# Optimization experiments

Measured on AMD Instinct MI355X. Metric: run time of the kernel, lower is better.

The kernel has to match this reference:

```python
import jax, jax.numpy as jnp
import numpy as np

B, D, M, H = 512, 2048, 128, 128
INIT_SCALE = 0.02

def setup_inputs() -> dict:
    key = jax.random.key(0)
    k_x, k_w1, k_w2 = jax.random.split(key, 3)
    return {
        "pre_activation_history": jax.random.normal(k_x, (B, D, M), dtype=jnp.float32),
        # conv1: grouped Conv1d(D -> D*H, kernel=M, groups=D) == per-channel W1[d]: [H, M]
        "W1": jax.random.normal(k_w1, (D, H, M), dtype=jnp.float32) * INIT_SCALE,
        "b1": jnp.zeros((D, H), dtype=jnp.float32),
        # linear_out: grouped 1x1 Conv1d(D*H -> D, groups=D) == per-channel w2[d]: [H]
        "W2": jax.random.normal(k_w2, (D, H), dtype=jnp.float32) * INIT_SCALE,
        "b2": jnp.zeros((D,), dtype=jnp.float32),
    }

def reference(pre_activation_history, W1, b1, W2, b2):
    # per-neuron MLP: [B,D,M] x [D,H,M] -> [B,D,H]
    h = jnp.einsum("bdm,dhm->bdh", pre_activation_history, W1) + b1
    g = jax.nn.gelu(h, approximate=False)  # torch F.gelu default = exact erf
    out = jnp.einsum("bdh,dh->bd", g, W2) + b2  # [B, D]
    return out
```

## Files before the change

kernel.cpp:

```cpp
#include <hip/hip_runtime.h>
#include <hip/hip_bf16.h>
#include <math.h>

#define B_SZ 512
#define D_SZ 2048
#define M_SZ 128
#define H_SZ 128
#define BCHUNK 64
#define NCHUNKS (B_SZ / BCHUNK)

typedef __attribute__((ext_vector_type(8))) short bf16x8;
typedef __attribute__((ext_vector_type(4))) float f32x4;
typedef __attribute__((ext_vector_type(4))) unsigned short us4;

__device__ __forceinline__ unsigned short f2bf(float f) {
    unsigned u = __builtin_bit_cast(unsigned, f);
    u += 0x7fffu + ((u >> 16) & 1u);
    return (unsigned short)(u >> 16);
}

__device__ __forceinline__ float gelu_fast(float h) {
    float u = h * h;
    float z = h * fmaf(0.0713548162726f, u, 1.5957691216057308f);
    float e = __expf(-z);
    return __fdividef(h, 1.0f + e);
}

__global__ __launch_bounds__(256, 3) void nlm_kernel(
    const float* __restrict__ x,
    const float* __restrict__ W1,
    const float* __restrict__ b1,
    const float* __restrict__ W2,
    const float* __restrict__ b2,
    float* __restrict__ out)
{
    __shared__ __align__(16) unsigned short W1s[H_SZ * M_SZ];
    __shared__ __align__(16) unsigned short Xs[BCHUNK * M_SZ];

    const int bid = blockIdx.x;
    const int d = (bid & 7) * 256 + (bid >> 3);

    const int tid  = threadIdx.x;
    const int l    = tid & 63;
    const int w    = tid >> 6;
    const int lrow = l & 15;
    const int lk   = l >> 4;
    const int swz  = (lrow & 7) << 4;

    const float* W1d = W1 + (size_t)d * (H_SZ * M_SZ);
    #pragma unroll
    for (int i = 0; i < 16; ++i) {
        int idx = tid + i * 256;
        int r = idx >> 5, c4 = idx & 31;
        const float4 v = *(const float4*)(W1d + (r << 7) + (c4 << 2));
        us4 u; u.x = f2bf(v.x); u.y = f2bf(v.y); u.z = f2bf(v.z); u.w = f2bf(v.w);
        int byte = (r << 8) + ((c4 << 3) ^ ((r & 7) << 4));
        *(us4*)((char*)W1s + byte) = u;
    }

    float w2r[8], b1r[8];
    #pragma unroll
    for (int n = 0; n < 8; ++n) {
        w2r[n] = W2[(size_t)d * H_SZ + n * 16 + lrow];
        b1r[n] = b1[(size_t)d * H_SZ + n * 16 + lrow];
    }
    const float b2v = b2[d];

    const int xr_row = tid >> 5;
    const int xr_c4  = tid & 31;
    float4 xr[8];
    #pragma unroll
    for (int i = 0; i < 8; ++i)
        xr[i] = *(const float4*)(x + ((size_t)(xr_row + i * 8) * D_SZ + d) * M_SZ + (xr_c4 << 2));

    for (int c = 0; c < NCHUNKS; ++c) {
        #pragma unroll
        for (int i = 0; i < 8; ++i) {
            int r = xr_row + i * 8;
            us4 u; u.x = f2bf(xr[i].x); u.y = f2bf(xr[i].y);
                   u.z = f2bf(xr[i].z); u.w = f2bf(xr[i].w);
            int byte = (r << 8) + ((xr_c4 << 3) ^ ((r & 7) << 4));
            *(us4*)((char*)Xs + byte) = u;
        }
        __syncthreads();

        if (c + 1 < NCHUNKS) {
            const size_t b0n = (size_t)(c + 1) * BCHUNK;
            #pragma unroll
            for (int i = 0; i < 8; ++i)
                xr[i] = *(const float4*)(x + ((b0n + xr_row + i * 8) * D_SZ + d) * M_SZ + (xr_c4 << 2));
        }

        f32x4 acc[8];
        #pragma unroll
        for (int n = 0; n < 8; ++n)
            acc[n] = (f32x4){0.f, 0.f, 0.f, 0.f};

        #pragma unroll
        for (int k = 0; k < 4; ++k) {
            const int colb = (k << 6) + (lk << 4);
            const int arow = w * 16 + lrow;
            bf16x8 a = *(const bf16x8*)((const char*)Xs + (arow << 8) + (colb ^ swz));
            bf16x8 bb[8];
            #pragma unroll
            for (int n = 0; n < 8; ++n) {
                int row = n * 16 + lrow;
                bb[n] = *(const bf16x8*)((const char*)W1s + (row << 8) + (colb ^ swz));
            }
            #pragma unroll
            for (int n = 0; n < 8; ++n)
                acc[n] = __builtin_amdgcn_mfma_f32_16x16x32_bf16(a, bb[n], acc[n], 0, 0, 0);
        }

        asm volatile("" ::: "memory");
        __builtin_amdgcn_sched_barrier(0);
        __builtin_amdgcn_s_barrier();
        __builtin_amdgcn_sched_barrier(0);
        asm volatile("" ::: "memory");

        float p[4] = {0.f, 0.f, 0.f, 0.f};
        #pragma unroll
        for (int n = 0; n < 8; ++n) {
            const float w2v = w2r[n];
            const float b1v = b1r[n];
            #pragma unroll
            for (int r = 0; r < 4; ++r) {
                float h = acc[n][r] + b1v;
                p[r] += gelu_fast(h) * w2v;
            }
        }

        #pragma unroll
        for (int off = 1; off < 16; off <<= 1)
            #pragma unroll
            for (int r = 0; r < 4; ++r)
                p[r] += __shfl_xor(p[r], off, 64);

        if (lrow == 0) {
            #pragma unroll
            for (int r = 0; r < 4; ++r)
                out[(size_t)(c * BCHUNK + w * 16 + lk * 4 + r) * D_SZ + d] = p[r] + b2v;
        }
    }
}

extern "C" void kernel_launch(void* const* d_in, const int* in_sizes, int n_in,
                              void* d_out, int out_size, void* d_ws, size_t ws_size,
                              hipStream_t stream) {
    const float* x  = (const float*)d_in[0];
    const float* W1 = (const float*)d_in[1];
    const float* b1 = (const float*)d_in[2];
    const float* W2 = (const float*)d_in[3];
    const float* b2 = (const float*)d_in[4];
    float* out = (float*)d_out;

    hipLaunchKernelGGL(nlm_kernel, dim3(D_SZ), dim3(256), 0, stream,
                       x, W1, b1, W2, b2, out);
}
```

Before: 152.3 us.

## Load X fragments directly into MFMA registers, drop X shared-memory staging

Each lane now loads its own MFMA A-operand slice of x straight from global memory into registers and converts it to bf16 in place. This removes the X shared-memory buffer, its swizzled stores, and both per-chunk block barriers. The cost is less coalesced global loads (each lane reads 32-byte pieces spread across rows), but it frees LDS and removes the synchronisation between waves inside the chunk loop.

```diff
diff --git a/kernel.cpp b/kernel.cpp
--- a/kernel.cpp
+++ b/kernel.cpp
@@ -35,7 +35,6 @@
     float* __restrict__ out)
 {
     __shared__ __align__(16) unsigned short W1s[H_SZ * M_SZ];
-    __shared__ __align__(16) unsigned short Xs[BCHUNK * M_SZ];
 
     const int bid = blockIdx.x;
     const int d = (bid & 7) * 256 + (bid >> 3);
@@ -66,29 +65,40 @@
     }
     const float b2v = b2[d];
 
-    const int xr_row = tid >> 5;
-    const int xr_c4  = tid & 31;
-    float4 xr[8];
+    const float* px = x + ((size_t)(w * 16 + lrow) * D_SZ + d) * M_SZ + lk * 8;
+    const size_t cstride = (size_t)BCHUNK * D_SZ * M_SZ;
+
+    float4 xa[8];
     #pragma unroll
-    for (int i = 0; i < 8; ++i)
-        xr[i] = *(const float4*)(x + ((size_t)(xr_row + i * 8) * D_SZ + d) * M_SZ + (xr_c4 << 2));
+    for (int k = 0; k < 4; ++k) {
+        xa[2 * k]     = *(const float4*)(px + k * 32);
+        xa[2 * k + 1] = *(const float4*)(px + k * 32 + 4);
+    }
+    const float* pnext = px + cstride;
+
+    __syncthreads();
 
     for (int c = 0; c < NCHUNKS; ++c) {
+        bf16x8 af[4];
         #pragma unroll
-        for (int i = 0; i < 8; ++i) {
-            int r = xr_row + i * 8;
-            us4 u; u.x = f2bf(xr[i].x); u.y = f2bf(xr[i].y);
-                   u.z = f2bf(xr[i].z); u.w = f2bf(xr[i].w);
-            int byte = (r << 8) + ((xr_c4 << 3) ^ ((r & 7) << 4));
-            *(us4*)((char*)Xs + byte) = u;
+        for (int k = 0; k < 4; ++k) {
+            af[k][0] = (short)f2bf(xa[2 * k].x);
+            af[k][1] = (short)f2bf(xa[2 * k].y);
+            af[k][2] = (short)f2bf(xa[2 * k].z);
+            af[k][3] = (short)f2bf(xa[2 * k].w);
+            af[k][4] = (short)f2bf(xa[2 * k + 1].x);
+            af[k][5] = (short)f2bf(xa[2 * k + 1].y);
+            af[k][6] = (short)f2bf(xa[2 * k + 1].z);
+            af[k][7] = (short)f2bf(xa[2 * k + 1].w);
         }
-        __syncthreads();
 
         if (c + 1 < NCHUNKS) {
-            const size_t b0n = (size_t)(c + 1) * BCHUNK;
             #pragma unroll
-            for (int i = 0; i < 8; ++i)
-                xr[i] = *(const float4*)(x + ((b0n + xr_row + i * 8) * D_SZ + d) * M_SZ + (xr_c4 << 2));
+            for (int k = 0; k < 4; ++k) {
+                xa[2 * k]     = *(const float4*)(pnext + k * 32);
+                xa[2 * k + 1] = *(const float4*)(pnext + k * 32 + 4);
+            }
+            pnext += cstride;
         }
 
         f32x4 acc[8];
@@ -99,24 +109,13 @@
         #pragma unroll
         for (int k = 0; k < 4; ++k) {
             const int colb = (k << 6) + (lk << 4);
-            const int arow = w * 16 + lrow;
-            bf16x8 a = *(const bf16x8*)((const char*)Xs + (arow << 8) + (colb ^ swz));
-            bf16x8 bb[8];
             #pragma unroll
             for (int n = 0; n < 8; ++n) {
-                int row = n * 16 + lrow;
-                bb[n] = *(const bf16x8*)((const char*)W1s + (row << 8) + (colb ^ swz));
+                bf16x8 bb = *(const bf16x8*)((const char*)W1s +
+                               ((n * 16 + lrow) << 8) + (colb ^ swz));
+                acc[n] = __builtin_amdgcn_mfma_f32_16x16x32_bf16(af[k], bb, acc[n], 0, 0, 0);
             }
-            #pragma unroll
-            for (int n = 0; n < 8; ++n)
-                acc[n] = __builtin_amdgcn_mfma_f32_16x16x32_bf16(a, bb[n], acc[n], 0, 0, 0);
         }
-
-        asm volatile("" ::: "memory");
-        __builtin_amdgcn_sched_barrier(0);
-        __builtin_amdgcn_s_barrier();
-        __builtin_amdgcn_sched_barrier(0);
-        asm volatile("" ::: "memory");
 
         float p[4] = {0.f, 0.f, 0.f, 0.f};
         #pragma unroll
```

Result: slower. 353.3 us (+132.0%).

## Give each wave a private X tile to remove per-chunk block barriers

Applied to the files above, without the earlier changes.

Each wave now loads, converts and stores only the 16 batch rows it consumes into its own LDS slice. This lets both the pre-MFMA __syncthreads and the post-MFMA s_barrier be dropped, leaving a single barrier after the W1 staging. Waves then run independently and can overlap their global loads, MFMAs and GELU epilogues. The trade is that each wave's loads now cover 16 rows with stride 2, which may change coalescing. Within a wave, the LDS write-then-read ordering has no barrier and depends on in-order wave execution and LDS wait counts.

```diff
diff --git a/kernel.cpp b/kernel.cpp
--- a/kernel.cpp
+++ b/kernel.cpp
@@ -6,6 +6,7 @@
 #define D_SZ 2048
 #define M_SZ 128
 #define H_SZ 128
+#define WROWS 16
 #define BCHUNK 64
 #define NCHUNKS (B_SZ / BCHUNK)
 
@@ -35,7 +36,7 @@
     float* __restrict__ out)
 {
     __shared__ __align__(16) unsigned short W1s[H_SZ * M_SZ];
-    __shared__ __align__(16) unsigned short Xs[BCHUNK * M_SZ];
+    __shared__ __align__(16) unsigned short Xs[4][WROWS * M_SZ];
 
     const int bid = blockIdx.x;
     const int d = (bid & 7) * 256 + (bid >> 3);
@@ -66,29 +67,36 @@
     }
     const float b2v = b2[d];
 
-    const int xr_row = tid >> 5;
-    const int xr_c4  = tid & 31;
+    const int xrow = l >> 5;
+    const int xc4  = l & 31;
+    unsigned short* myXs = &Xs[w][0];
+
+    const float* px0 = x + ((size_t)(w * WROWS + xrow) * D_SZ + d) * M_SZ + (xc4 << 2);
+    const size_t rstride = (size_t)2 * D_SZ * M_SZ;
+    const size_t cstride = (size_t)BCHUNK * D_SZ * M_SZ;
     float4 xr[8];
     #pragma unroll
     for (int i = 0; i < 8; ++i)
-        xr[i] = *(const float4*)(x + ((size_t)(xr_row + i * 8) * D_SZ + d) * M_SZ + (xr_c4 << 2));
+        xr[i] = *(const float4*)(px0 + i * rstride);
+    const float* pnext = px0 + cstride;
+
+    __syncthreads();
 
     for (int c = 0; c < NCHUNKS; ++c) {
         #pragma unroll
         for (int i = 0; i < 8; ++i) {
-            int r = xr_row + i * 8;
+            int r = xrow + i * 2;
             us4 u; u.x = f2bf(xr[i].x); u.y = f2bf(xr[i].y);
                    u.z = f2bf(xr[i].z); u.w = f2bf(xr[i].w);
-            int byte = (r << 8) + ((xr_c4 << 3) ^ ((r & 7) << 4));
-            *(us4*)((char*)Xs + byte) = u;
+            int byte = (r << 8) + ((xc4 << 3) ^ ((r & 7) << 4));
+            *(us4*)((char*)myXs + byte) = u;
         }
-        __syncthreads();
 
         if (c + 1 < NCHUNKS) {
-            const size_t b0n = (size_t)(c + 1) * BCHUNK;
             #pragma unroll
             for (int i = 0; i < 8; ++i)
-                xr[i] = *(const float4*)(x + ((b0n + xr_row + i * 8) * D_SZ + d) * M_SZ + (xr_c4 << 2));
+                xr[i] = *(const float4*)(pnext + i * rstride);
+            pnext += cstride;
         }
 
         f32x4 acc[8];
@@ -99,24 +107,14 @@
         #pragma unroll
         for (int k = 0; k < 4; ++k) {
             const int colb = (k << 6) + (lk << 4);
-            const int arow = w * 16 + lrow;
-            bf16x8 a = *(const bf16x8*)((const char*)Xs + (arow << 8) + (colb ^ swz));
-            bf16x8 bb[8];
+            bf16x8 a = *(const bf16x8*)((const char*)myXs + (lrow << 8) + (colb ^ swz));
             #pragma unroll
             for (int n = 0; n < 8; ++n) {
-                int row = n * 16 + lrow;
-                bb[n] = *(const bf16x8*)((const char*)W1s + (row << 8) + (colb ^ swz));
+                bf16x8 bb = *(const bf16x8*)((const char*)W1s +
+                               ((n * 16 + lrow) << 8) + (colb ^ swz));
+                acc[n] = __builtin_amdgcn_mfma_f32_16x16x32_bf16(a, bb, acc[n], 0, 0, 0);
             }
-            #pragma unroll
-            for (int n = 0; n < 8; ++n)
-                acc[n] = __builtin_amdgcn_mfma_f32_16x16x32_bf16(a, bb[n], acc[n], 0, 0, 0);
         }
-
-        asm volatile("" ::: "memory");
-        __builtin_amdgcn_sched_barrier(0);
-        __builtin_amdgcn_s_barrier();
-        __builtin_amdgcn_sched_barrier(0);
-        asm volatile("" ::: "memory");
 
         float p[4] = {0.f, 0.f, 0.f, 0.f};
         #pragma unroll
@@ -139,7 +137,7 @@
         if (lrow == 0) {
             #pragma unroll
             for (int r = 0; r < 4; ++r)
-                out[(size_t)(c * BCHUNK + w * 16 + lk * 4 + r) * D_SZ + d] = p[r] + b2v;
+                out[(size_t)(c * BCHUNK + w * WROWS + lk * 4 + r) * D_SZ + d] = p[r] + b2v;
         }
     }
 }
```

Measured after the change: 284.6 us. 1.87x slower.

## Stream x into LDS via async global_load_lds double buffering with split-H waves

Applied to the files above, without the earlier changes.

Replaces the register-staged x loads and bf16 conversion with direct global-to-LDS async loads (fp32) into two buffers, prefetching two chunks ahead and synchronising with explicit vmcnt waits. Chunk size drops to 32 and the four waves are split 2x2 over batch rows and H halves, with partial sums combined through LDS. Outputs are buffered in LDS and written once at the end. The intent is to hide global load latency and free registers, at the cost of doubled LDS footprint (fp32 x), per-read conversion, extra barriers, and lower occupancy (launch bounds 2).

```diff
diff --git a/kernel.cpp b/kernel.cpp
--- a/kernel.cpp
+++ b/kernel.cpp
@@ -6,7 +6,7 @@
 #define D_SZ 2048
 #define M_SZ 128
 #define H_SZ 128
-#define BCHUNK 64
+#define BCHUNK 32
 #define NCHUNKS (B_SZ / BCHUNK)
 
 typedef __attribute__((ext_vector_type(8))) short bf16x8;
@@ -26,7 +26,26 @@
     return __fdividef(h, 1.0f + e);
 }
 
-__global__ __launch_bounds__(256, 3) void nlm_kernel(
+__device__ __forceinline__ void lds_barrier() {
+    __builtin_amdgcn_sched_barrier(0);
+    asm volatile("s_waitcnt lgkmcnt(0)" ::: "memory");
+    __builtin_amdgcn_sched_barrier(0);
+    __builtin_amdgcn_s_barrier();
+    __builtin_amdgcn_sched_barrier(0);
+}
+
+__device__ __forceinline__ void wait_vm4() {
+    __builtin_amdgcn_sched_barrier(0);
+    asm volatile("s_waitcnt vmcnt(4)" ::: "memory");
+    __builtin_amdgcn_sched_barrier(0);
+}
+__device__ __forceinline__ void wait_vm0() {
+    __builtin_amdgcn_sched_barrier(0);
+    asm volatile("s_waitcnt vmcnt(0)" ::: "memory");
+    __builtin_amdgcn_sched_barrier(0);
+}
+
+__global__ __launch_bounds__(256, 2) void nlm_kernel(
     const float* __restrict__ x,
     const float* __restrict__ W1,
     const float* __restrict__ b1,
@@ -35,7 +54,9 @@
     float* __restrict__ out)
 {
     __shared__ __align__(16) unsigned short W1s[H_SZ * M_SZ];
-    __shared__ __align__(16) unsigned short Xs[BCHUNK * M_SZ];
+    __shared__ __align__(16) float Xs[2][BCHUNK * M_SZ];
+    __shared__ float red[2][BCHUNK];
+    __shared__ float outLDS[B_SZ];
 
     const int bid = blockIdx.x;
     const int d = (bid & 7) * 256 + (bid >> 3);
@@ -43,9 +64,11 @@
     const int tid  = threadIdx.x;
     const int l    = tid & 63;
     const int w    = tid >> 6;
+    const int wr   = w >> 1;
+    const int wc   = w & 1;
     const int lrow = l & 15;
     const int lk   = l >> 4;
-    const int swz  = (lrow & 7) << 4;
+    const int swz16 = (lrow & 7) << 4;
 
     const float* W1d = W1 + (size_t)d * (H_SZ * M_SZ);
     #pragma unroll
@@ -58,78 +81,75 @@
         *(us4*)((char*)W1s + byte) = u;
     }
 
-    float w2r[8], b1r[8];
+    float w2r[4], b1r[4];
     #pragma unroll
-    for (int n = 0; n < 8; ++n) {
-        w2r[n] = W2[(size_t)d * H_SZ + n * 16 + lrow];
-        b1r[n] = b1[(size_t)d * H_SZ + n * 16 + lrow];
+    for (int n = 0; n < 4; ++n) {
+        int hh = wc * 64 + n * 16 + lrow;
+        w2r[n] = W2[(size_t)d * H_SZ + hh];
+        b1r[n] = b1[(size_t)d * H_SZ + hh];
     }
     const float b2v = b2[d];
 
-    const int xr_row = tid >> 5;
-    const int xr_c4  = tid & 31;
-    float4 xr[8];
-    #pragma unroll
-    for (int i = 0; i < 8; ++i)
-        xr[i] = *(const float4*)(x + ((size_t)(xr_row + i * 8) * D_SZ + d) * M_SZ + (xr_c4 << 2));
+    wait_vm0();
+
+    const char* xb = (const char*)x;
+    auto stage = [&](int c, int buf) {
+        #pragma unroll
+        for (int j = 0; j < 4; ++j) {
+            int rl  = w * 8 + j * 2 + (l >> 5);
+            int col = ((l & 31) << 4) ^ ((rl & 7) << 4);
+            const void* src = xb + ((size_t)(c * BCHUNK + rl) * D_SZ + d) * (M_SZ * 4) + col;
+            void* dst = (char*)&Xs[buf][0] + (size_t)(w * 8 + j * 2) * 512;
+            __builtin_amdgcn_global_load_lds(
+                (const __attribute__((address_space(1))) void*)src,
+                (__attribute__((address_space(3))) void*)dst, 16, 0, 0);
+        }
+    };
+
+    stage(0, 0);
+    stage(1, 1);
 
     for (int c = 0; c < NCHUNKS; ++c) {
+        if (c == NCHUNKS - 1) wait_vm0(); else wait_vm4();
+        lds_barrier();
+
+        const char* xbuf = (const char*)&Xs[c & 1][0];
+
+        f32x4 acc[4];
         #pragma unroll
-        for (int i = 0; i < 8; ++i) {
-            int r = xr_row + i * 8;
-            us4 u; u.x = f2bf(xr[i].x); u.y = f2bf(xr[i].y);
-                   u.z = f2bf(xr[i].z); u.w = f2bf(xr[i].w);
-            int byte = (r << 8) + ((xr_c4 << 3) ^ ((r & 7) << 4));
-            *(us4*)((char*)Xs + byte) = u;
-        }
-        __syncthreads();
-
-        if (c + 1 < NCHUNKS) {
-            const size_t b0n = (size_t)(c + 1) * BCHUNK;
-            #pragma unroll
-            for (int i = 0; i < 8; ++i)
-                xr[i] = *(const float4*)(x + ((b0n + xr_row + i * 8) * D_SZ + d) * M_SZ + (xr_c4 << 2));
-        }
-
-        f32x4 acc[8];
-        #pragma unroll
-        for (int n = 0; n < 8; ++n)
-            acc[n] = (f32x4){0.f, 0.f, 0.f, 0.f};
+        for (int n = 0; n < 4; ++n) acc[n] = (f32x4){0.f, 0.f, 0.f, 0.f};
 
         #pragma unroll
         for (int k = 0; k < 4; ++k) {
-            const int colb = (k << 6) + (lk << 4);
-            const int arow = w * 16 + lrow;
-            bf16x8 a = *(const bf16x8*)((const char*)Xs + (arow << 8) + (colb ^ swz));
-            bf16x8 bb[8];
+            const int R  = wr * 16 + lrow;
+            const int sw = (R & 7) << 4;
+            const int cb = (k << 7) + (lk << 5);
+            const char* base = xbuf + (R << 9);
+            f32x4 x0 = *(const f32x4*)(base + (cb ^ sw));
+            f32x4 x1 = *(const f32x4*)(base + ((cb + 16) ^ sw));
+            bf16x8 af;
+            af[0] = (short)f2bf(x0[0]); af[1] = (short)f2bf(x0[1]);
+            af[2] = (short)f2bf(x0[2]); af[3] = (short)f2bf(x0[3]);
+            af[4] = (short)f2bf(x1[0]); af[5] = (short)f2bf(x1[1]);
+            af[6] = (short)f2bf(x1[2]); af[7] = (short)f2bf(x1[3]);
+            const int wcol = ((k << 6) | (lk << 4)) ^ swz16;
             #pragma unroll
-            for (int n = 0; n < 8; ++n) {
-                int row = n * 16 + lrow;
-                bb[n] = *(const bf16x8*)((const char*)W1s + (row << 8) + (colb ^ swz));
+            for (int n = 0; n < 4; ++n) {
+                int rowW = wc * 64 + n * 16 + lrow;
+                bf16x8 bb = *(const bf16x8*)((const char*)W1s + (rowW << 8) + wcol);
+                acc[n] = __builtin_amdgcn_mfma_f32_16x16x32_bf16(af, bb, acc[n], 0, 0, 0);
             }
-            #pragma unroll
-            for (int n = 0; n < 8; ++n)
-                acc[n] = __builtin_amdgcn_mfma_f32_16x16x32_bf16(a, bb[n], acc[n], 0, 0, 0);
         }
-
-        asm volatile("" ::: "memory");
-        __builtin_amdgcn_sched_barrier(0);
-        __builtin_amdgcn_s_barrier();
-        __builtin_amdgcn_sched_barrier(0);
-        asm volatile("" ::: "memory");
 
         float p[4] = {0.f, 0.f, 0.f, 0.f};
         #pragma unroll
-        for (int n = 0; n < 8; ++n) {
+        for (int n = 0; n < 4; ++n) {
             const float w2v = w2r[n];
             const float b1v = b1r[n];
             #pragma unroll
-            for (int r = 0; r < 4; ++r) {
-                float h = acc[n][r] + b1v;
-                p[r] += gelu_fast(h) * w2v;
-            }
+            for (int r = 0; r < 4; ++r)
+                p[r] += gelu_fast(acc[n][r] + b1v) * w2v;
         }
-
         #pragma unroll
         for (int off = 1; off < 16; off <<= 1)
             #pragma unroll
@@ -139,9 +159,20 @@
         if (lrow == 0) {
             #pragma unroll
             for (int r = 0; r < 4; ++r)
-                out[(size_t)(c * BCHUNK + w * 16 + lk * 4 + r) * D_SZ + d] = p[r] + b2v;
+                red[wc][wr * 16 + lk * 4 + r] = p[r];
         }
+
+        lds_barrier();
+
+        if (c + 2 < NCHUNKS) stage(c + 2, c & 1);
+
+        if (tid < BCHUNK)
+            outLDS[c * BCHUNK + tid] = red[0][tid] + red[1][tid] + b2v;
     }
+
+    lds_barrier();
+    out[(size_t)tid * D_SZ + d]         = outLDS[tid];
+    out[(size_t)(tid + 256) * D_SZ + d] = outLDS[tid + 256];
 }
 
 extern "C" void kernel_launch(void* const* d_in, const int* in_sizes, int n_in,
```

Result: slower. 190.0 us (+24.8%).
